# Kernel tuning notes

Measured on AMD Instinct MI355X. Metric: run time of the kernel, lower is better.

## Reference

```python
import jax, jax.numpy as jnp
import numpy as np

D_MODEL = 1024
D_STATE = 16


def setup_inputs() -> dict:
    key = jax.random.key(0)
    k1, k2, k3 = jax.random.split(key, 3)
    x = jax.random.normal(k1, (8, 4096, D_MODEL), dtype=jnp.float32)
    alpha = jax.random.normal(k2, (D_MODEL, D_STATE), dtype=jnp.float32) * 0.02
    delta = jax.random.normal(k3, (D_MODEL, D_STATE), dtype=jnp.float32) * 0.02
    gamma = jnp.ones((D_MODEL,), dtype=jnp.float32)
    beta = jnp.zeros((D_MODEL,), dtype=jnp.float32)
    return {"x": x, "alpha": alpha, "delta": delta, "gamma": gamma, "beta": beta}


def reference(x, alpha, delta, gamma, beta):
    # x: [B, L, D]; alpha/delta: [D, N]; gamma/beta: [D]
    B, L, D = x.shape
    a = jax.nn.sigmoid(alpha)   # [D, N]
    d = jax.nn.sigmoid(delta)   # [D, N]

    def step(h, xt):
        # h: [B, D, N], xt: [B, D]
        h = a * h + (1.0 - a) * xt[..., None]
        y = jnp.einsum('bdn,dn->bd', h, d)
        return h, y

    h0 = jnp.zeros((B, D, a.shape[-1]), dtype=x.dtype)
    # scan over time axis: move L to leading dim
    _, ys = jax.lax.scan(step, h0, jnp.swapaxes(x, 0, 1))  # ys: [L, B, D]
    y = jnp.swapaxes(ys, 0, 1)  # [B, L, D]
    return y * gamma + beta
```

## Files before the change

### kernel.cpp

```cpp
#include <hip/hip_runtime.h>
#include <cmath>

#define D_MODEL 1024
#define D_STATE 16
#define BATCH   8
#define SEQLEN  4096
#define CHUNK   64
#define WARM    32
#define NCHUNK  (SEQLEN / CHUNK)
#define TROWS   8
#define TFLOATS (TROWS * D_MODEL)

__global__ __launch_bounds__(1024, 4) void ema_kernel(
    const float* __restrict__ x,
    const float* __restrict__ alpha,
    const float* __restrict__ delta,
    const float* __restrict__ gamma,
    const float* __restrict__ beta,
    float* __restrict__ out)
{
    __shared__ float xb[TFLOATS];
    __shared__ float yb[TFLOATS];

    const int tid = threadIdx.x;
    const int b   = blockIdx.x & (BATCH - 1);
    const int c   = blockIdx.x >> 3;

    float a[D_STATE], e[D_STATE], z[D_STATE];
    #pragma unroll
    for (int n = 0; n < D_STATE; ++n) {
        const float al = alpha[tid * D_STATE + n];
        const float de = delta[tid * D_STATE + n];
        const float an = 1.0f / (1.0f + __expf(-al));
        const float dn = 1.0f / (1.0f + __expf(-de));
        a[n] = an;
        e[n] = dn * (1.0f - an);
        z[n] = 0.0f;
    }

    const int t0     = c * CHUNK;
    const int wsteps = (c == 0) ? 0 : WARM;
    const int ntiles = (wsteps + CHUNK) / TROWS;
    const int wtiles = wsteps / TROWS;

    const float* xg = x   + ((size_t)b * SEQLEN + (t0 - wsteps)) * D_MODEL;
    float*       og = out + ((size_t)b * SEQLEN + t0) * D_MODEL;
    const float gm = gamma[tid];
    const float bt = beta[tid];

    const int so0 = 4 * tid;
    const int so1 = TFLOATS / 2 + so0;

    float4 r0 = *(const float4*)(xg + so0);
    float4 r1 = *(const float4*)(xg + so1);

    for (int k = 0; k < ntiles; ++k) {
        *(float4*)(xb + so0) = r0;
        *(float4*)(xb + so1) = r1;
        if (k + 1 < ntiles) {
            const float* gt = xg + (size_t)(k + 1) * TFLOATS;
            r0 = *(const float4*)(gt + so0);
            r1 = *(const float4*)(gt + so1);
        }
        __syncthreads();
        if (k < wtiles) {
            #pragma unroll
            for (int i = 0; i < TROWS; ++i) {
                const float xv = xb[i * D_MODEL + tid];
                #pragma unroll
                for (int n = 0; n < D_STATE; ++n)
                    z[n] = fmaf(a[n], z[n], xv);
            }
            __syncthreads();
        } else {
            #pragma unroll
            for (int i = 0; i < TROWS; ++i) {
                const float xv = xb[i * D_MODEL + tid];
                float y0 = 0.f, y1 = 0.f, y2 = 0.f, y3 = 0.f;
                #pragma unroll
                for (int n = 0; n < D_STATE; n += 4) {
                    z[n+0] = fmaf(a[n+0], z[n+0], xv); y0 = fmaf(z[n+0], e[n+0], y0);
                    z[n+1] = fmaf(a[n+1], z[n+1], xv); y1 = fmaf(z[n+1], e[n+1], y1);
                    z[n+2] = fmaf(a[n+2], z[n+2], xv); y2 = fmaf(z[n+2], e[n+2], y2);
                    z[n+3] = fmaf(a[n+3], z[n+3], xv); y3 = fmaf(z[n+3], e[n+3], y3);
                }
                yb[i * D_MODEL + tid] = fmaf((y0 + y1) + (y2 + y3), gm, bt);
            }
            __syncthreads();
            float* ot = og + (size_t)(k * TROWS - wsteps) * D_MODEL;
            *(float4*)(ot + so0) = *(const float4*)(yb + so0);
            *(float4*)(ot + so1) = *(const float4*)(yb + so1);
        }
    }
}

extern "C" void kernel_launch(void* const* d_in, const int* in_sizes, int n_in,
                              void* d_out, int out_size, void* d_ws, size_t ws_size,
                              hipStream_t stream) {
    const float* x     = (const float*)d_in[0];
    const float* alpha = (const float*)d_in[1];
    const float* delta = (const float*)d_in[2];
    const float* gamma = (const float*)d_in[3];
    const float* beta  = (const float*)d_in[4];
    float* out = (float*)d_out;

    ema_kernel<<<dim3(BATCH * NCHUNK), dim3(1024), 0, stream>>>(
        x, alpha, delta, gamma, beta, out);
}
```

Baseline: 262.1 us.

## Deepen global prefetch to four tiles with double-buffered LDS and direct output stores

Each block now prefetches four tiles of x into registers ahead of use and double-buffers them in shared memory, so one barrier per tile separates the write of the next tile from the compute on the current one. The output staging buffer is removed and each thread stores its result directly to global memory with a coalesced per-row store. The chunk size is doubled, which halves the grid and lowers the share of time spent on warm-up steps, but leaves fewer blocks to fill the GPU. The deeper prefetch holds more registers per thread, and the hand-placed waitcnt and sched_barrier rely on the compiler not reordering memory operations around them.

```diff
diff --git a/kernel.cpp b/kernel.cpp
--- a/kernel.cpp
+++ b/kernel.cpp
@@ -5,11 +5,12 @@
 #define D_STATE 16
 #define BATCH   8
 #define SEQLEN  4096
-#define CHUNK   64
+#define CHUNK   128
 #define WARM    32
 #define NCHUNK  (SEQLEN / CHUNK)
 #define TROWS   8
 #define TFLOATS (TROWS * D_MODEL)
+#define DEPTH   4
 
 __global__ __launch_bounds__(1024, 4) void ema_kernel(
     const float* __restrict__ x,
@@ -19,8 +20,7 @@
     const float* __restrict__ beta,
     float* __restrict__ out)
 {
-    __shared__ float xb[TFLOATS];
-    __shared__ float yb[TFLOATS];
+    __shared__ float xb[2][TFLOATS];
 
     const int tid = threadIdx.x;
     const int b   = blockIdx.x & (BATCH - 1);
@@ -42,56 +42,82 @@
     const int wsteps = (c == 0) ? 0 : WARM;
     const int ntiles = (wsteps + CHUNK) / TROWS;
     const int wtiles = wsteps / TROWS;
+    const int nm     = ntiles / 4;
 
     const float* xg = x   + ((size_t)b * SEQLEN + (t0 - wsteps)) * D_MODEL;
-    float*       og = out + ((size_t)b * SEQLEN + t0) * D_MODEL;
+    float*       og = out + ((size_t)b * SEQLEN + t0) * D_MODEL + tid;
     const float gm = gamma[tid];
     const float bt = beta[tid];
 
     const int so0 = 4 * tid;
     const int so1 = TFLOATS / 2 + so0;
 
-    float4 r0 = *(const float4*)(xg + so0);
-    float4 r1 = *(const float4*)(xg + so1);
+    float4 ra0, rb0, ra1, rb1, ra2, rb2, ra3, rb3;
 
-    for (int k = 0; k < ntiles; ++k) {
-        *(float4*)(xb + so0) = r0;
-        *(float4*)(xb + so1) = r1;
-        if (k + 1 < ntiles) {
-            const float* gt = xg + (size_t)(k + 1) * TFLOATS;
-            r0 = *(const float4*)(gt + so0);
-            r1 = *(const float4*)(gt + so1);
-        }
-        __syncthreads();
-        if (k < wtiles) {
-            #pragma unroll
-            for (int i = 0; i < TROWS; ++i) {
-                const float xv = xb[i * D_MODEL + tid];
-                #pragma unroll
-                for (int n = 0; n < D_STATE; ++n)
-                    z[n] = fmaf(a[n], z[n], xv);
-            }
-            __syncthreads();
-        } else {
-            #pragma unroll
-            for (int i = 0; i < TROWS; ++i) {
-                const float xv = xb[i * D_MODEL + tid];
-                float y0 = 0.f, y1 = 0.f, y2 = 0.f, y3 = 0.f;
-                #pragma unroll
-                for (int n = 0; n < D_STATE; n += 4) {
-                    z[n+0] = fmaf(a[n+0], z[n+0], xv); y0 = fmaf(z[n+0], e[n+0], y0);
-                    z[n+1] = fmaf(a[n+1], z[n+1], xv); y1 = fmaf(z[n+1], e[n+1], y1);
-                    z[n+2] = fmaf(a[n+2], z[n+2], xv); y2 = fmaf(z[n+2], e[n+2], y2);
-                    z[n+3] = fmaf(a[n+3], z[n+3], xv); y3 = fmaf(z[n+3], e[n+3], y3);
-                }
-                yb[i * D_MODEL + tid] = fmaf((y0 + y1) + (y2 + y3), gm, bt);
-            }
-            __syncthreads();
-            float* ot = og + (size_t)(k * TROWS - wsteps) * D_MODEL;
-            *(float4*)(ot + so0) = *(const float4*)(yb + so0);
-            *(float4*)(ot + so1) = *(const float4*)(yb + so1);
-        }
+#define ISSUE(RA, RB, t) { \
+    const float* gt = xg + (size_t)(t) * TFLOATS; \
+    RA = *(const float4*)(gt + so0); \
+    RB = *(const float4*)(gt + so1); }
+
+#define DSWRITE(RA, RB, s) { \
+    *(float4*)(&xb[s][so0]) = RA; \
+    *(float4*)(&xb[s][so1]) = RB; }
+
+#define BAR() { \
+    asm volatile("s_waitcnt lgkmcnt(0)" ::: "memory"); \
+    __builtin_amdgcn_sched_barrier(0); \
+    __builtin_amdgcn_s_barrier(); }
+
+#define CONSUME(kk) { \
+    const float* lb = xb[(kk) & 1]; \
+    if ((kk) < wtiles) { \
+        _Pragma("unroll") \
+        for (int i = 0; i < TROWS; ++i) { \
+            const float xv = lb[i * D_MODEL + tid]; \
+            _Pragma("unroll") \
+            for (int n = 0; n < D_STATE; ++n) \
+                z[n] = fmaf(a[n], z[n], xv); \
+        } \
+    } else { \
+        float* op = og + (size_t)((kk) * TROWS - wsteps) * D_MODEL; \
+        _Pragma("unroll") \
+        for (int i = 0; i < TROWS; ++i) { \
+            const float xv = lb[i * D_MODEL + tid]; \
+            float y0 = 0.f, y1 = 0.f, y2 = 0.f, y3 = 0.f; \
+            _Pragma("unroll") \
+            for (int n = 0; n < D_STATE; n += 4) { \
+                z[n+0] = fmaf(a[n+0], z[n+0], xv); y0 = fmaf(z[n+0], e[n+0], y0); \
+                z[n+1] = fmaf(a[n+1], z[n+1], xv); y1 = fmaf(z[n+1], e[n+1], y1); \
+                z[n+2] = fmaf(a[n+2], z[n+2], xv); y2 = fmaf(z[n+2], e[n+2], y2); \
+                z[n+3] = fmaf(a[n+3], z[n+3], xv); y3 = fmaf(z[n+3], e[n+3], y3); \
+            } \
+            op[i * D_MODEL] = fmaf((y0 + y1) + (y2 + y3), gm, bt); \
+        } \
+    } }
+
+#define STEP(j, RAc, RBc, RAn, RBn) { \
+    const int k = 4 * m + (j); \
+    if (k + DEPTH < ntiles) ISSUE(RAc, RBc, k + DEPTH) \
+    BAR() \
+    if (k + 1 < ntiles) DSWRITE(RAn, RBn, ((j) + 1) & 1) \
+    CONSUME(k) }
+
+    ISSUE(ra0, rb0, 0) ISSUE(ra1, rb1, 1) ISSUE(ra2, rb2, 2) ISSUE(ra3, rb3, 3)
+    DSWRITE(ra0, rb0, 0)
+
+    #pragma unroll 1
+    for (int m = 0; m < nm; ++m) {
+        STEP(0, ra0, rb0, ra1, rb1)
+        STEP(1, ra1, rb1, ra2, rb2)
+        STEP(2, ra2, rb2, ra3, rb3)
+        STEP(3, ra3, rb3, ra0, rb0)
     }
+
+#undef ISSUE
+#undef DSWRITE
+#undef BAR
+#undef CONSUME
+#undef STEP
 }
 
 extern "C" void kernel_launch(void* const* d_in, const int* in_sizes, int n_in,
```

Measured after the change: 288.9 us. 1.1x slower.
